# Performance work log

Measured on AMD Instinct MI355X. Metric: run time of the kernel, lower is better.

The kernel has to match this reference:

```python
import jax, jax.numpy as jnp
import numpy as np

EMBED_DIM = 512
K = 30
B, M, L = 64, 1024, 256

def setup_inputs() -> dict:
    key = jax.random.key(0)
    ks = jax.random.split(key, 7)
    s = 0.05  # small scale so tanh/softmax stay in a sane numeric range
    return {
        "V": jax.random.normal(ks[0], (B, EMBED_DIM, M), dtype=jnp.float32),
        "Q": jax.random.normal(ks[1], (B, L, EMBED_DIM), dtype=jnp.float32),
        "W_b": jax.random.normal(ks[2], (EMBED_DIM, EMBED_DIM), dtype=jnp.float32) * s,
        "W_v": jax.random.normal(ks[3], (K, EMBED_DIM), dtype=jnp.float32) * s,
        "W_q": jax.random.normal(ks[4], (K, EMBED_DIM), dtype=jnp.float32) * s,
        "w_hv": jax.random.normal(ks[5], (K, 1), dtype=jnp.float32) * s,
        "w_hq": jax.random.normal(ks[6], (K, 1), dtype=jnp.float32) * s,
    }

def reference(V, Q, W_b, W_v, W_q, w_hv, w_hq):
    # V: [B, d, M], Q: [B, L, d]
    b, d, m = V.shape
    l = Q.shape[1]
    WbV = jnp.einsum('de,bem->bdm', W_b, V)          # [B, d, M]
    C = jnp.matmul(Q, WbV)                            # affinity [B, L, M]
    WvV = jnp.einsum('kd,bdm->bkm', W_v, V)           # [B, k, M]
    WqQ = jnp.einsum('kd,bld->bkl', W_q, Q)           # [B, k, L]
    H_v = jnp.tanh(WvV + jnp.matmul(WqQ, C))          # [B, k, M]
    H_q = jnp.tanh(WqQ + jnp.matmul(WvV, jnp.swapaxes(C, 1, 2)))  # [B, k, L]
    a_v = jax.nn.softmax(jnp.einsum('ko,bkm->bom', w_hv, H_v), axis=2)  # [B, 1, M]
    a_q = jax.nn.softmax(jnp.einsum('ko,bkl->bol', w_hq, H_q), axis=2)  # [B, 1, L]
    # torch stacks a_v M times then matmuls -> M identical pooled rows; compute
    # the pooled vector once and broadcast (same math, no [B,M,M] intermediate).
    v1 = jnp.matmul(a_v, jnp.swapaxes(V, 1, 2))       # [B, 1, d]
    q1 = jnp.matmul(a_q, Q)                           # [B, 1, d]
    v = jnp.broadcast_to(v1, (b, m, d))               # [B, M, d]
    q = jnp.broadcast_to(q1, (b, l, d))               # [B, L, d]
    return (v, q)
```

## Files before the change

kernel.cpp:

```cpp
#include <hip/hip_runtime.h>

constexpr int Bn = 64;
constexpr int Dn = 512;
constexpr int Mn = 1024;
constexpr int Ln = 256;
constexpr int Kn = 30;
constexpr int KP = 32;

typedef __attribute__((ext_vector_type(4))) float f32x4;
typedef __attribute__((ext_vector_type(2))) float f32x2;
typedef __attribute__((ext_vector_type(4))) unsigned int u32x4;
typedef __attribute__((ext_vector_type(8))) _Float16 f16x8;
typedef __attribute__((ext_vector_type(2))) _Float16 f16x2;
typedef unsigned short ushort_t;

__device__ __forceinline__ void cvt_pair(float a, float b,
                                         unsigned int& hp, unsigned int& lp)
{
    _Float16 ha = (_Float16)a, hb = (_Float16)b;
    _Float16 la = (_Float16)(a - (float)ha), lb = (_Float16)(b - (float)hb);
    f16x2 hv = {ha, hb}, lv = {la, lb};
    hp = __builtin_bit_cast(unsigned int, hv);
    lp = __builtin_bit_cast(unsigned int, lv);
}

__device__ __forceinline__ unsigned int cvt_one_pack(float x)
{
    _Float16 h = (_Float16)x;
    _Float16 l = (_Float16)(x - (float)h);
    return (unsigned int)__builtin_bit_cast(ushort_t, l) |
           ((unsigned int)__builtin_bit_cast(ushort_t, h) << 16);
}

template <int MT, bool BT, int EPI>
__global__ __launch_bounds__(256) void fgemm_kernel(
    const float* __restrict__ A, const float* __restrict__ B,
    float* __restrict__ C,
    const float* __restrict__ Wvec, const float* __restrict__ Xadd,
    float* __restrict__ Yout,
    int Mreal, int Ndim, int Kdim, int ldA, int ldB,
    long sA, long sB, long sC)
{
    constexpr int BM = MT * 16;
    constexpr int AP = 20;
    constexpr int ASZ = BM * AP;
    constexpr int BP_NN = 66;
    constexpr int BSZ = BT ? (2 * 64 * AP) : (32 * BP_NN);
    __shared__ unsigned int smem[2 * ASZ + BSZ];
    __shared__ float wsh[32];
    unsigned int* Ah = smem;
    unsigned int* Al = smem + ASZ;
    unsigned int* Bh = smem + 2 * ASZ;
    unsigned int* Bl = Bh + 64 * AP;
    unsigned int* Bp = smem + 2 * ASZ;

    const int t  = threadIdx.x;
    const int n0 = blockIdx.x * 64;
    const int m0 = blockIdx.y * BM;
    const int b  = blockIdx.z;
    const float* Ab = A + (long)b * sA;
    const float* Bb = B + (long)b * sB;

    const int lane = t & 63, w = t >> 6;
    const int fr = lane & 15, g = lane >> 4;
    const int kp  = t & 15, r16 = t >> 4;
    const int nn  = t & 63, kr  = t >> 6;

    if (EPI >= 2 && t < 32) wsh[t] = (t < Kn) ? Wvec[t] : 0.f;

    float as[MT][2];
    float bsv[8];

    auto stageA = [&](int k0) {
        #pragma unroll
        for (int i = 0; i < MT; i++) {
            int gm = m0 + r16 + 16 * i;
            float x0 = 0.f, x1 = 0.f;
            if (gm < Mreal) {
                f32x2 v = *(const f32x2*)&Ab[(long)gm * ldA + k0 + 2 * kp];
                x0 = v.x; x1 = v.y;
            }
            as[i][0] = x0; as[i][1] = x1;
        }
    };
    auto stageB = [&](int k0) {
        if constexpr (BT) {
            #pragma unroll
            for (int i = 0; i < 4; i++) {
                f32x2 v = *(const f32x2*)&Bb[(long)(n0 + r16 + 16 * i) * ldB + k0 + 2 * kp];
                bsv[2 * i] = v.x; bsv[2 * i + 1] = v.y;
            }
        } else {
            #pragma unroll
            for (int i = 0; i < 8; i++)
                bsv[i] = Bb[(long)(k0 + kr + 4 * i) * ldB + n0 + nn];
        }
    };
    auto storeStage = [&]() {
        #pragma unroll
        for (int i = 0; i < MT; i++) {
            unsigned int hp, lp;
            cvt_pair(as[i][0], as[i][1], hp, lp);
            Ah[(r16 + 16 * i) * AP + kp] = hp;
            Al[(r16 + 16 * i) * AP + kp] = lp;
        }
        if constexpr (BT) {
            #pragma unroll
            for (int i = 0; i < 4; i++) {
                unsigned int hp, lp;
                cvt_pair(bsv[2 * i], bsv[2 * i + 1], hp, lp);
                Bh[(r16 + 16 * i) * AP + kp] = hp;
                Bl[(r16 + 16 * i) * AP + kp] = lp;
            }
        } else {
            #pragma unroll
            for (int i = 0; i < 8; i++)
                Bp[(kr + 4 * i) * BP_NN + nn] = cvt_one_pack(bsv[i]);
        }
    };

    f32x4 acc[MT];
    #pragma unroll
    for (int i = 0; i < MT; i++) acc[i] = (f32x4){0.f, 0.f, 0.f, 0.f};

    auto computeTile = [&]() {
        f16x8 fbh, fbl;
        if constexpr (BT) {
            int row = w * 16 + fr;
            fbh = __builtin_bit_cast(f16x8, *(const u32x4*)&Bh[row * AP + g * 4]);
            fbl = __builtin_bit_cast(f16x8, *(const u32x4*)&Bl[row * AP + g * 4]);
        } else {
            unsigned int p[8];
            #pragma unroll
            for (int j = 0; j < 8; j++)
                p[j] = Bp[(g * 8 + j) * BP_NN + w * 16 + fr];
            unsigned int hu[4], lu[4];
            #pragma unroll
            for (int r = 0; r < 4; r++) {
                hu[r] = __builtin_amdgcn_perm(p[2 * r + 1], p[2 * r], 0x07060302u);
                lu[r] = __builtin_amdgcn_perm(p[2 * r + 1], p[2 * r], 0x05040100u);
            }
            fbh = __builtin_bit_cast(f16x8, (u32x4){hu[0], hu[1], hu[2], hu[3]});
            fbl = __builtin_bit_cast(f16x8, (u32x4){lu[0], lu[1], lu[2], lu[3]});
        }
        #pragma unroll
        for (int mt = 0; mt < MT; mt++) {
            int row = fr + 16 * mt;
            f16x8 fah = __builtin_bit_cast(f16x8, *(const u32x4*)&Ah[row * AP + g * 4]);
            f16x8 fal = __builtin_bit_cast(f16x8, *(const u32x4*)&Al[row * AP + g * 4]);
            acc[mt] = __builtin_amdgcn_mfma_f32_16x16x32_f16(fah, fbh, acc[mt], 0, 0, 0);
            acc[mt] = __builtin_amdgcn_mfma_f32_16x16x32_f16(fal, fbh, acc[mt], 0, 0, 0);
            acc[mt] = __builtin_amdgcn_mfma_f32_16x16x32_f16(fah, fbl, acc[mt], 0, 0, 0);
        }
    };

    stageA(0); stageB(0);
    storeStage();
    __syncthreads();
    const int nt = Kdim >> 5;
    for (int tt = 0; tt < nt; tt++) {
        const bool more = (tt + 1 < nt);
        if (more) { stageA((tt + 1) * 32); stageB((tt + 1) * 32); }
        computeTile();
        if (more) {
            __syncthreads();
            storeStage();
            __syncthreads();
        }
    }

    const int col = n0 + w * 16 + fr;
    if constexpr (EPI == 0) {
        float* Cb = C + (long)b * sC;
        #pragma unroll
        for (int mt = 0; mt < MT; mt++)
            #pragma unroll
            for (int r = 0; r < 4; r++)
                Cb[(long)(m0 + mt * 16 + g * 4 + r) * Ndim + col] = acc[mt][r];
    } else if constexpr (EPI == 1) {
        #pragma unroll
        for (int mt = 0; mt < MT; mt++)
            #pragma unroll
            for (int r = 0; r < 4; r++) {
                int gr = m0 + mt * 16 + g * 4 + r;
                int sr = (gr >> 5) * 64 + 32 + (gr & 31);
                C[(long)sr * Ndim + col] = acc[mt][r];
            }
    } else if constexpr (EPI == 2) {
        float* Cb = C + (long)b * sC;
        float s = 0.f;
        #pragma unroll
        for (int mt = 0; mt < 2; mt++)
            #pragma unroll
            for (int r = 0; r < 4; r++) {
                int row = mt * 16 + g * 4 + r;
                Cb[(long)row * Ndim + col] = acc[mt][r];
                s += wsh[row] * tanhf(acc[mt][r] + acc[mt + 2][r]);
            }
        s += __shfl_xor(s, 16, 64);
        s += __shfl_xor(s, 32, 64);
        if (g == 0) Yout[(long)b * Ndim + col] = s;
    } else {
        const float* Xb = Xadd + (long)b * sC;
        float s = 0.f;
        #pragma unroll
        for (int mt = 0; mt < MT; mt++)
            #pragma unroll
            for (int r = 0; r < 4; r++) {
                int row = mt * 16 + g * 4 + r;
                s += wsh[row] * tanhf(Xb[(long)row * Ndim + col] + acc[mt][r]);
            }
        s += __shfl_xor(s, 16, 64);
        s += __shfl_xor(s, 32, 64);
        if (g == 0) Yout[(long)b * Ndim + col] = s;
    }
}

__global__ void prep_sa_kernel(const float* __restrict__ Wv,
                               float* __restrict__ Sa)
{
    const int b = blockIdx.x, t = threadIdx.x;
    for (int idx = t; idx < 32 * Dn; idx += 256) {
        int row = idx >> 9, col = idx & 511;
        Sa[((long)b * 64 + row) * Dn + col] =
            (row < Kn) ? Wv[(long)row * Dn + col] : 0.f;
    }
}

__global__ __launch_bounds__(1024) void smpool_v_kernel(
    const float* __restrict__ sv, const float* __restrict__ V,
    float* __restrict__ v1)
{
    const int b = blockIdx.y, qtr = blockIdx.x, t = threadIdx.x;
    const int wid = t >> 6, lane = t & 63;
    __shared__ float red[16];
    __shared__ float bc;
    __shared__ float av[Mn];

    float x = sv[(long)b * Mn + t];
    float v = x;
    #pragma unroll
    for (int off = 32; off > 0; off >>= 1) v = fmaxf(v, __shfl_down(v, off, 64));
    if (lane == 0) red[wid] = v;
    __syncthreads();
    if (t == 0) {
        float m = red[0];
        for (int i = 1; i < 16; i++) m = fmaxf(m, red[i]);
        bc = m;
    }
    __syncthreads();
    float e = expf(x - bc);
    v = e;
    #pragma unroll
    for (int off = 32; off > 0; off >>= 1) v += __shfl_down(v, off, 64);
    if (lane == 0) red[wid] = v;
    __syncthreads();
    if (t == 0) {
        float s = 0.f;
        for (int i = 0; i < 16; i++) s += red[i];
        bc = s;
    }
    __syncthreads();
    av[t] = e / bc;
    __syncthreads();

    f32x4 aa[4];
    #pragma unroll
    for (int i = 0; i < 4; i++) aa[i] = *(const f32x4*)&av[4 * (lane + 64 * i)];

    #pragma unroll
    for (int j = 0; j < 8; j++) {
        int e_ = qtr * 128 + wid * 8 + j;
        const float* vr = V + ((long)b * Dn + e_) * Mn;
        float acc = 0.f;
        #pragma unroll
        for (int i = 0; i < 4; i++) {
            f32x4 vv = *(const f32x4*)&vr[4 * (lane + 64 * i)];
            acc += vv.x * aa[i].x + vv.y * aa[i].y + vv.z * aa[i].z + vv.w * aa[i].w;
        }
        #pragma unroll
        for (int off = 32; off > 0; off >>= 1) acc += __shfl_down(acc, off, 64);
        if (lane == 0) v1[(long)b * Dn + e_] = acc;
    }
}

__global__ __launch_bounds__(256) void smpool_q_kernel(
    const float* __restrict__ sq, const float* __restrict__ Q,
    float* __restrict__ q1)
{
    const int b = blockIdx.y, half = blockIdx.x, t = threadIdx.x;
    const int wid = t >> 6, lane = t & 63;
    __shared__ float red[4];
    __shared__ float bc;
    __shared__ float aq[Ln];

    float x = sq[(long)b * Ln + t];
    float v = x;
    #pragma unroll
    for (int off = 32; off > 0; off >>= 1) v = fmaxf(v, __shfl_down(v, off, 64));
    if (lane == 0) red[wid] = v;
    __syncthreads();
    if (t == 0) {
        float m = red[0];
        for (int i = 1; i < 4; i++) m = fmaxf(m, red[i]);
        bc = m;
    }
    __syncthreads();
    float e = expf(x - bc);
    v = e;
    #pragma unroll
    for (int off = 32; off > 0; off >>= 1) v += __shfl_down(v, off, 64);
    if (lane == 0) red[wid] = v;
    __syncthreads();
    if (t == 0) {
        float s = 0.f;
        for (int i = 0; i < 4; i++) s += red[i];
        bc = s;
    }
    __syncthreads();
    aq[t] = e / bc;
    __syncthreads();

    const int e_ = half * 256 + t;
    const float* Qb = Q + (long)b * Ln * Dn;
    float acc = 0.f;
    #pragma unroll 4
    for (int l = 0; l < Ln; l++)
        acc += aq[l] * Qb[(long)l * Dn + e_];
    q1[(long)b * Dn + e_] = acc;
}

__global__ void bcast_kernel(const float* __restrict__ v1,
                             const float* __restrict__ q1,
                             float* __restrict__ out)
{
    const long nv4 = (long)Bn * Mn * Dn / 4;
    const long nq4 = (long)Bn * Ln * Dn / 4;
    long idx = (long)blockIdx.x * blockDim.x + threadIdx.x;
    float4* o4 = (float4*)out;
    if (idx < nv4) {
        long fidx = idx * 4;
        int e4 = (int)(fidx & (Dn - 1));
        long bm = fidx >> 9;
        int b = (int)(bm >> 10);
        o4[idx] = *(const float4*)(v1 + (long)b * Dn + e4);
    } else if (idx < nv4 + nq4) {
        long fidx = (idx - nv4) * 4;
        int e4 = (int)(fidx & (Dn - 1));
        long bl = fidx >> 9;
        int b = (int)(bl >> 8);
        o4[idx] = *(const float4*)(q1 + (long)b * Dn + e4);
    }
}


extern "C" void kernel_launch(void* const* d_in, const int* in_sizes, int n_in,
                              void* d_out, int out_size, void* d_ws, size_t ws_size,
                              hipStream_t stream)
{
    const float* V    = (const float*)d_in[0];
    const float* Q    = (const float*)d_in[1];
    const float* W_b  = (const float*)d_in[2];
    const float* W_v  = (const float*)d_in[3];
    const float* W_q  = (const float*)d_in[4];
    const float* w_hv = (const float*)d_in[5];
    const float* w_hq = (const float*)d_in[6];
    float* out = (float*)d_out;

    const long szWqQ = (long)Bn * KP * Ln;
    const long szU   = (long)Bn * KP * Dn;
    const long szSa  = (long)Bn * 64 * Dn;
    const long szSo  = (long)Bn * 32 * Mn;

    float* ws   = (float*)d_ws;
    float* WqQ  = ws;
    float* U    = WqQ + szWqQ;
    float* Sa   = U   + szU;
    float* Sout = Sa  + szSa;
    float* R    = Sout + szSo;
    float* G    = R   + szU;
    float* sv   = G   + szU;
    float* sq   = sv  + (long)Bn * Mn;
    float* v1   = sq  + (long)Bn * Ln;
    float* q1   = v1  + (long)Bn * Dn;

    prep_sa_kernel<<<Bn, 256, 0, stream>>>(W_v, Sa);

    fgemm_kernel<2, true, 0><<<dim3(Ln / 64, 1, Bn), 256, 0, stream>>>(
        W_q, Q, WqQ, nullptr, nullptr, nullptr,
        Kn, Ln, Dn, Dn, Dn, 0, (long)Ln * Dn, (long)KP * Ln);

    fgemm_kernel<2, false, 0><<<dim3(Dn / 64, 1, Bn), 256, 0, stream>>>(
        WqQ, Q, U, nullptr, nullptr, nullptr,
        KP, Dn, Ln, Ln, Dn, (long)KP * Ln, (long)Ln * Dn, (long)KP * Dn);

    fgemm_kernel<4, false, 1><<<dim3(Dn / 64, Bn * KP / 64, 1), 256, 0, stream>>>(
        U, W_b, Sa, nullptr, nullptr, nullptr,
        Bn * KP, Dn, Dn, Dn, Dn, 0, 0, 0);

    fgemm_kernel<4, false, 2><<<dim3(Mn / 64, 1, Bn), 256, 0, stream>>>(
        Sa, V, Sout, w_hv, nullptr, sv,
        64, Mn, Dn, Dn, Mn, (long)64 * Dn, (long)Dn * Mn, (long)32 * Mn);

    fgemm_kernel<2, true, 0><<<dim3(Dn / 64, 1, Bn), 256, 0, stream>>>(
        Sout, V, R, nullptr, nullptr, nullptr,
        KP, Dn, Mn, Mn, Mn, (long)32 * Mn, (long)Dn * Mn, (long)KP * Dn);

    fgemm_kernel<4, true, 0><<<dim3(Dn / 64, Bn * KP / 64, 1), 256, 0, stream>>>(
        R, W_b, G, nullptr, nullptr, nullptr,
        Bn * KP, Dn, Dn, Dn, Dn, 0, 0, 0);

    fgemm_kernel<2, true, 3><<<dim3(Ln / 64, 1, Bn), 256, 0, stream>>>(
        G, Q, nullptr, w_hq, WqQ, sq,
        KP, Ln, Dn, Dn, Dn, (long)KP * Dn, (long)Ln * Dn, (long)KP * Ln);

    smpool_v_kernel<<<dim3(4, Bn), 1024, 0, stream>>>(sv, V, v1);

    smpool_q_kernel<<<dim3(2, Bn), 256, 0, stream>>>(sq, Q, q1);

    {
        long n4 = (long)Bn * Mn * Dn / 4 + (long)Bn * Ln * Dn / 4;
        bcast_kernel<<<(int)((n4 + 255) / 256), 256, 0, stream>>>(v1, q1, out);
    }
}
```

Baseline: 494.6 us.

## Split-K the small GEMMs into two slabs and sum partials in consumer loads

Adds a split-K template parameter so most GEMM launches run two K halves as separate blocks. Each half writes its partial to its own slab, and the next kernel adds the two slabs while loading its A operand or epilogue input. The prep_sa kernel and the EPI==1 scatter are dropped: the W_v rows are read directly and the U·W_b partials come from a second pointer. smpool_q also spreads the L reduction over more blocks with a shuffle reduce. The aim is more blocks on the GPU for these small-batch GEMMs, at the cost of extra partial-buffer traffic and doubled A loads.

```diff
diff --git a/kernel.cpp b/kernel.cpp
--- a/kernel.cpp
+++ b/kernel.cpp
@@ -32,14 +32,16 @@
            ((unsigned int)__builtin_bit_cast(ushort_t, h) << 16);
 }
 
-template <int MT, bool BT, int EPI>
+template <int MT, bool BT, int EPI, int KS, int ASRC, bool XSUM>
 __global__ __launch_bounds__(256) void fgemm_kernel(
     const float* __restrict__ A, const float* __restrict__ B,
+    const float* __restrict__ A2,
     float* __restrict__ C,
     const float* __restrict__ Wvec, const float* __restrict__ Xadd,
     float* __restrict__ Yout,
     int Mreal, int Ndim, int Kdim, int ldA, int ldB,
-    long sA, long sB, long sC)
+    long sA, long sB, long sC,
+    long sASlab, long slabC, long sXslab)
 {
     constexpr int BM = MT * 16;
     constexpr int AP = 20;
@@ -56,7 +58,8 @@
 
     const int t  = threadIdx.x;
     const int n0 = blockIdx.x * 64;
-    const int m0 = blockIdx.y * BM;
+    const int mb = blockIdx.y / KS, ks = blockIdx.y % KS;
+    const int m0 = mb * BM;
     const int b  = blockIdx.z;
     const float* Ab = A + (long)b * sA;
     const float* Bb = B + (long)b * sB;
@@ -66,6 +69,10 @@
     const int kp  = t & 15, r16 = t >> 4;
     const int nn  = t & 63, kr  = t >> 6;
 
+    const int kLen = Kdim / KS;
+    const int k00  = ks * kLen;
+    const int nt   = kLen >> 5;
+
     if (EPI >= 2 && t < 32) wsh[t] = (t < Kn) ? Wvec[t] : 0.f;
 
     float as[MT][2];
@@ -76,9 +83,28 @@
         for (int i = 0; i < MT; i++) {
             int gm = m0 + r16 + 16 * i;
             float x0 = 0.f, x1 = 0.f;
-            if (gm < Mreal) {
-                f32x2 v = *(const f32x2*)&Ab[(long)gm * ldA + k0 + 2 * kp];
-                x0 = v.x; x1 = v.y;
+            if constexpr (ASRC == 2) {
+                if (gm < Kn) {
+                    f32x2 v = *(const f32x2*)&A[(long)gm * ldA + k0 + 2 * kp];
+                    x0 = v.x; x1 = v.y;
+                } else if (gm >= 32) {
+                    const float* p = &A2[((long)b * 32 + gm - 32) * ldA + k0 + 2 * kp];
+                    f32x2 v  = *(const f32x2*)p;
+                    f32x2 v2 = *(const f32x2*)(p + sASlab);
+                    x0 = v.x + v2.x; x1 = v.y + v2.y;
+                }
+            } else if constexpr (ASRC == 1) {
+                if (gm < Mreal) {
+                    const float* p = &Ab[(long)gm * ldA + k0 + 2 * kp];
+                    f32x2 v  = *(const f32x2*)p;
+                    f32x2 v2 = *(const f32x2*)(p + sASlab);
+                    x0 = v.x + v2.x; x1 = v.y + v2.y;
+                }
+            } else {
+                if (gm < Mreal) {
+                    f32x2 v = *(const f32x2*)&Ab[(long)gm * ldA + k0 + 2 * kp];
+                    x0 = v.x; x1 = v.y;
+                }
             }
             as[i][0] = x0; as[i][1] = x1;
         }
@@ -154,13 +180,12 @@
         }
     };
 
-    stageA(0); stageB(0);
+    stageA(k00); stageB(k00);
     storeStage();
     __syncthreads();
-    const int nt = Kdim >> 5;
     for (int tt = 0; tt < nt; tt++) {
         const bool more = (tt + 1 < nt);
-        if (more) { stageA((tt + 1) * 32); stageB((tt + 1) * 32); }
+        if (more) { stageA(k00 + (tt + 1) * 32); stageB(k00 + (tt + 1) * 32); }
         computeTile();
         if (more) {
             __syncthreads();
@@ -171,21 +196,12 @@
 
     const int col = n0 + w * 16 + fr;
     if constexpr (EPI == 0) {
-        float* Cb = C + (long)b * sC;
+        float* Cb = C + (long)ks * slabC + (long)b * sC;
         #pragma unroll
         for (int mt = 0; mt < MT; mt++)
             #pragma unroll
             for (int r = 0; r < 4; r++)
                 Cb[(long)(m0 + mt * 16 + g * 4 + r) * Ndim + col] = acc[mt][r];
-    } else if constexpr (EPI == 1) {
-        #pragma unroll
-        for (int mt = 0; mt < MT; mt++)
-            #pragma unroll
-            for (int r = 0; r < 4; r++) {
-                int gr = m0 + mt * 16 + g * 4 + r;
-                int sr = (gr >> 5) * 64 + 32 + (gr & 31);
-                C[(long)sr * Ndim + col] = acc[mt][r];
-            }
     } else if constexpr (EPI == 2) {
         float* Cb = C + (long)b * sC;
         float s = 0.f;
@@ -208,22 +224,13 @@
             #pragma unroll
             for (int r = 0; r < 4; r++) {
                 int row = mt * 16 + g * 4 + r;
-                s += wsh[row] * tanhf(Xb[(long)row * Ndim + col] + acc[mt][r]);
+                float x = Xb[(long)row * Ndim + col];
+                if constexpr (XSUM) x += Xb[sXslab + (long)row * Ndim + col];
+                s += wsh[row] * tanhf(x + acc[mt][r]);
             }
         s += __shfl_xor(s, 16, 64);
         s += __shfl_xor(s, 32, 64);
         if (g == 0) Yout[(long)b * Ndim + col] = s;
-    }
-}
-
-__global__ void prep_sa_kernel(const float* __restrict__ Wv,
-                               float* __restrict__ Sa)
-{
-    const int b = blockIdx.x, t = threadIdx.x;
-    for (int idx = t; idx < 32 * Dn; idx += 256) {
-        int row = idx >> 9, col = idx & 511;
-        Sa[((long)b * 64 + row) * Dn + col] =
-            (row < Kn) ? Wv[(long)row * Dn + col] : 0.f;
     }
 }
 
@@ -288,7 +295,7 @@
     const float* __restrict__ sq, const float* __restrict__ Q,
     float* __restrict__ q1)
 {
-    const int b = blockIdx.y, half = blockIdx.x, t = threadIdx.x;
+    const int b = blockIdx.y, eb = blockIdx.x, t = threadIdx.x;
     const int wid = t >> 6, lane = t & 63;
     __shared__ float red[4];
     __shared__ float bc;
@@ -321,13 +328,17 @@
     aq[t] = e / bc;
     __syncthreads();
 
-    const int e_ = half * 256 + t;
+    const int e_ = eb * 64 + (t >> 2), qtr = t & 3;
     const float* Qb = Q + (long)b * Ln * Dn;
     float acc = 0.f;
     #pragma unroll 4
-    for (int l = 0; l < Ln; l++)
+    for (int i = 0; i < 64; i++) {
+        int l = qtr * 64 + i;
         acc += aq[l] * Qb[(long)l * Dn + e_];
-    q1[(long)b * Dn + e_] = acc;
+    }
+    acc += __shfl_xor(acc, 1, 64);
+    acc += __shfl_xor(acc, 2, 64);
+    if (qtr == 0) q1[(long)b * Dn + e_] = acc;
 }
 
 __global__ void bcast_kernel(const float* __restrict__ v1,
@@ -369,54 +380,65 @@
 
     const long szWqQ = (long)Bn * KP * Ln;
     const long szU   = (long)Bn * KP * Dn;
-    const long szSa  = (long)Bn * 64 * Dn;
     const long szSo  = (long)Bn * 32 * Mn;
 
     float* ws   = (float*)d_ws;
-    float* WqQ  = ws;
-    float* U    = WqQ + szWqQ;
-    float* Sa   = U   + szU;
-    float* Sout = Sa  + szSa;
-    float* R    = Sout + szSo;
-    float* G    = R   + szU;
-    float* sv   = G   + szU;
-    float* sq   = sv  + (long)Bn * Mn;
-    float* v1   = sq  + (long)Bn * Ln;
-    float* q1   = v1  + (long)Bn * Dn;
-
-    prep_sa_kernel<<<Bn, 256, 0, stream>>>(W_v, Sa);
-
-    fgemm_kernel<2, true, 0><<<dim3(Ln / 64, 1, Bn), 256, 0, stream>>>(
-        W_q, Q, WqQ, nullptr, nullptr, nullptr,
-        Kn, Ln, Dn, Dn, Dn, 0, (long)Ln * Dn, (long)KP * Ln);
-
-    fgemm_kernel<2, false, 0><<<dim3(Dn / 64, 1, Bn), 256, 0, stream>>>(
-        WqQ, Q, U, nullptr, nullptr, nullptr,
-        KP, Dn, Ln, Ln, Dn, (long)KP * Ln, (long)Ln * Dn, (long)KP * Dn);
-
-    fgemm_kernel<4, false, 1><<<dim3(Dn / 64, Bn * KP / 64, 1), 256, 0, stream>>>(
-        U, W_b, Sa, nullptr, nullptr, nullptr,
-        Bn * KP, Dn, Dn, Dn, Dn, 0, 0, 0);
-
-    fgemm_kernel<4, false, 2><<<dim3(Mn / 64, 1, Bn), 256, 0, stream>>>(
-        Sa, V, Sout, w_hv, nullptr, sv,
-        64, Mn, Dn, Dn, Mn, (long)64 * Dn, (long)Dn * Mn, (long)32 * Mn);
-
-    fgemm_kernel<2, true, 0><<<dim3(Dn / 64, 1, Bn), 256, 0, stream>>>(
-        Sout, V, R, nullptr, nullptr, nullptr,
-        KP, Dn, Mn, Mn, Mn, (long)32 * Mn, (long)Dn * Mn, (long)KP * Dn);
-
-    fgemm_kernel<4, true, 0><<<dim3(Dn / 64, Bn * KP / 64, 1), 256, 0, stream>>>(
-        R, W_b, G, nullptr, nullptr, nullptr,
-        Bn * KP, Dn, Dn, Dn, Dn, 0, 0, 0);
-
-    fgemm_kernel<2, true, 3><<<dim3(Ln / 64, 1, Bn), 256, 0, stream>>>(
-        G, Q, nullptr, w_hq, WqQ, sq,
-        KP, Ln, Dn, Dn, Dn, (long)KP * Dn, (long)Ln * Dn, (long)KP * Ln);
+    float* WqQ2 = ws;
+    float* U2   = WqQ2 + 2 * szWqQ;
+    float* P2   = U2   + 2 * szU;
+    float* Sout = P2   + 2 * szU;
+    float* R2   = Sout + szSo;
+    float* G2   = R2   + 2 * szU;
+    float* sv   = G2   + 2 * szU;
+    float* sq   = sv   + (long)Bn * Mn;
+    float* v1   = sq   + (long)Bn * Ln;
+    float* q1   = v1   + (long)Bn * Dn;
+
+    fgemm_kernel<2, true, 0, 2, 0, false><<<dim3(4, 2, 64), 256, 0, stream>>>(
+        W_q, Q, nullptr, WqQ2, nullptr, nullptr, nullptr,
+        Kn, Ln, Dn, Dn, Dn,
+        0, (long)Ln * Dn, (long)KP * Ln,
+        0, szWqQ, 0);
+
+    fgemm_kernel<2, false, 0, 2, 1, false><<<dim3(8, 2, 64), 256, 0, stream>>>(
+        WqQ2, Q, nullptr, U2, nullptr, nullptr, nullptr,
+        KP, Dn, Ln, Ln, Dn,
+        (long)KP * Ln, (long)Ln * Dn, (long)KP * Dn,
+        szWqQ, szU, 0);
+
+    fgemm_kernel<4, false, 0, 2, 1, false><<<dim3(8, 64, 1), 256, 0, stream>>>(
+        U2, W_b, nullptr, P2, nullptr, nullptr, nullptr,
+        Bn * KP, Dn, Dn, Dn, Dn,
+        0, 0, 0,
+        szU, szU, 0);
+
+    fgemm_kernel<4, false, 2, 1, 2, false><<<dim3(16, 1, 64), 256, 0, stream>>>(
+        W_v, V, P2, Sout, w_hv, nullptr, sv,
+        64, Mn, Dn, Dn, Mn,
+        0, (long)Dn * Mn, (long)32 * Mn,
+        szU, 0, 0);
+
+    fgemm_kernel<2, true, 0, 2, 0, false><<<dim3(8, 2, 64), 256, 0, stream>>>(
+        Sout, V, nullptr, R2, nullptr, nullptr, nullptr,
+        KP, Dn, Mn, Mn, Mn,
+        (long)32 * Mn, (long)Dn * Mn, (long)KP * Dn,
+        0, szU, 0);
+
+    fgemm_kernel<4, true, 0, 2, 1, false><<<dim3(8, 64, 1), 256, 0, stream>>>(
+        R2, W_b, nullptr, G2, nullptr, nullptr, nullptr,
+        Bn * KP, Dn, Dn, Dn, Dn,
+        0, 0, 0,
+        szU, szU, 0);
+
+    fgemm_kernel<2, true, 3, 1, 1, true><<<dim3(4, 1, 64), 256, 0, stream>>>(
+        G2, Q, nullptr, nullptr, w_hq, WqQ2, sq,
+        KP, Ln, Dn, Dn, Dn,
+        (long)KP * Dn, (long)Ln * Dn, (long)KP * Ln,
+        szU, 0, szWqQ);
 
     smpool_v_kernel<<<dim3(4, Bn), 1024, 0, stream>>>(sv, V, v1);
 
-    smpool_q_kernel<<<dim3(2, Bn), 256, 0, stream>>>(sq, Q, q1);
+    smpool_q_kernel<<<dim3(8, Bn), 256, 0, stream>>>(sq, Q, q1);
 
     {
         long n4 = (long)Bn * Mn * Dn / 4 + (long)Bn * Ln * Dn / 4;
```

Result: faster. 457.2 us (-7.6%).
